# Performance work log

Measured on AMD Instinct MI355X. Metric: run time of the kernel, lower is better.

The kernel has to match this reference:

```python
import jax, jax.numpy as jnp
import numpy as np

N = 50000          # num graph nodes
E = 800000         # edges per direction
NGRAM, ODIM = 4, 32
DIMS = [128, 128, 64]
CLASSES = 128
MAXPE = 10
L2_EPS = 1e-12


def setup_inputs() -> dict:
    key = jax.random.key(0)
    ks = iter(jax.random.split(key, 40))
    d = {}
    d['x'] = jax.random.normal(next(ks), (N, DIMS[0]), jnp.float32)
    d['edge_index_in'] = jax.random.randint(next(ks), (2, E), 0, N, dtype=jnp.int64)
    d['edge_weight_in'] = jax.random.uniform(next(ks), (E,), jnp.float32)
    d['edge_index_out'] = jax.random.randint(next(ks), (2, E), 0, N, dtype=jnp.int64)
    d['edge_weight_out'] = jax.random.uniform(next(ks), (E,), jnp.float32)
    d['pe_table'] = jax.random.normal(next(ks), (MAXPE, ODIM), jnp.float32) * 0.05
    # per-layer DirectGCNLayer params (weights stored [in,out], i.e. torch W.T)
    for l in range(2):
        di, do = DIMS[l], DIMS[l + 1]
        s = 1.0 / np.sqrt(di)
        d[f'W_main_in_{l}'] = jax.random.normal(next(ks), (di, do), jnp.float32) * s
        d[f'W_main_out_{l}'] = jax.random.normal(next(ks), (di, do), jnp.float32) * s
        d[f'W_shared_{l}'] = jax.random.normal(next(ks), (di, do), jnp.float32) * s
        d[f'b_main_in_{l}'] = jnp.zeros((do,), jnp.float32)
        d[f'b_main_out_{l}'] = jnp.zeros((do,), jnp.float32)
        d[f'b_shared_in_{l}'] = jnp.zeros((do,), jnp.float32)
        d[f'b_shared_out_{l}'] = jnp.zeros((do,), jnp.float32)
        d[f'C_in_{l}'] = jnp.ones((N, 1), jnp.float32)
        d[f'C_out_{l}'] = jnp.ones((N, 1), jnp.float32)
    # residual projection for layer 1 (128 -> 64); layer 0 is identity
    d['res_W_1'] = jax.random.normal(next(ks), (DIMS[1], DIMS[2]), jnp.float32) * (1.0 / np.sqrt(DIMS[1]))
    d['res_b_1'] = jnp.zeros((DIMS[2],), jnp.float32)
    d['dec_W'] = jax.random.normal(next(ks), (DIMS[2], CLASSES), jnp.float32) * (1.0 / np.sqrt(DIMS[2]))
    d['dec_b'] = jnp.zeros((CLASSES,), jnp.float32)
    return d


def _prop(xW, ei, ew):
    # gather source, scale by edge weight, scatter-add to target (PyG aggr='add')
    return jax.ops.segment_sum(ew[:, None] * xW[ei[0]], ei[1], num_segments=N)


def _layer(h, ei_in, ew_in, ei_out, ew_out,
           Wmi, Wmo, Ws, bmi, bmo, bsi, bso, cin, cout):
    xs = h @ Ws  # shared transform, propagated over both edge sets
    ic = _prop(h @ Wmi, ei_in, ew_in) + bmi + _prop(xs, ei_in, ew_in) + bsi
    oc = _prop(h @ Wmo, ei_out, ew_out) + bmo + _prop(xs, ei_out, ew_out) + bso
    return cin * ic + cout * oc


def reference(x, edge_index_in, edge_weight_in, edge_index_out, edge_weight_out,
              pe_table,
              W_main_in_0, W_main_out_0, W_shared_0, b_main_in_0, b_main_out_0,
              b_shared_in_0, b_shared_out_0, C_in_0, C_out_0,
              W_main_in_1, W_main_out_1, W_shared_1, b_main_in_1, b_main_out_1,
              b_shared_in_1, b_shared_out_1, C_in_1, C_out_1,
              res_W_1, res_b_1, dec_W, dec_b):
    # positional encoding: add pe[:n_gram_len] to each n-gram slot
    h = (x.reshape(N, NGRAM, ODIM) + pe_table[:NGRAM][None]).reshape(N, NGRAM * ODIM)
    # layer 0 (identity residual); dropout p=0 / eval -> no-op
    h = jnp.tanh(_layer(h, edge_index_in, edge_weight_in, edge_index_out, edge_weight_out,
                        W_main_in_0, W_main_out_0, W_shared_0, b_main_in_0, b_main_out_0,
                        b_shared_in_0, b_shared_out_0, C_in_0, C_out_0) + h)
    # layer 1 (linear residual projection 128 -> 64)
    h = jnp.tanh(_layer(h, edge_index_in, edge_weight_in, edge_index_out, edge_weight_out,
                        W_main_in_1, W_main_out_1, W_shared_1, b_main_in_1, b_main_out_1,
                        b_shared_in_1, b_shared_out_1, C_in_1, C_out_1)
                 + h @ res_W_1 + res_b_1)
    logits = h @ dec_W + dec_b
    logp = jax.nn.log_softmax(logits, axis=-1)
    emb = h / (jnp.linalg.norm(h, axis=1, keepdims=True) + L2_EPS)
    return logp, emb
```

## Files before the change

### kernel.cpp

```cpp
#include <hip/hip_runtime.h>
#include <hip/hip_bf16.h>
#include <math.h>

typedef __hip_bfloat16  bf16;
typedef __hip_bfloat162 bf162;
typedef __attribute__((ext_vector_type(8))) short short8;
typedef __attribute__((ext_vector_type(4))) float floatx4;

#define BSZ     128
#define NBMAX   512
#define PACHUNK 8192

__device__ inline float4 bf4_to_f4(uint2 v) {
  float2 lo = __bfloat1622float2(*(bf162*)&v.x);
  float2 hi = __bfloat1622float2(*(bf162*)&v.y);
  return make_float4(lo.x, lo.y, hi.x, hi.y);
}
__device__ inline uint2 f4_to_bf4(float4 v) {
  bf162 lo = __float22bfloat162_rn(make_float2(v.x, v.y));
  bf162 hi = __float22bfloat162_rn(make_float2(v.z, v.w));
  uint2 r;
  r.x = *(unsigned*)&lo;
  r.y = *(unsigned*)&hi;
  return r;
}

__global__ __launch_bounds__(256) void k_bhist(const int* __restrict__ eiIn, const int* __restrict__ eiOut,
                                               int E, int* __restrict__ bcnt, int NB) {
  __shared__ int h[NBMAX];
  const int t = threadIdx.x;
  const int set = blockIdx.y;
  const int* dst = (set ? eiOut : eiIn) + E;
  for (int i = t; i < NB; i += 256) h[i] = 0;
  __syncthreads();
  const int base = blockIdx.x * PACHUNK;
  const int m = min(PACHUNK, E - base);
  #pragma unroll 4
  for (int r = 0; r < PACHUNK / 256; ++r) {
    int i = r * 256 + t;
    if (i < m) atomicAdd(&h[dst[base + i] >> 7], 1);
  }
  __syncthreads();
  for (int i = t; i < NB; i += 256) {
    int c = h[i];
    if (c) atomicAdd(&bcnt[set * NBMAX + i], c);
  }
}

__global__ __launch_bounds__(64) void k_bscan(const int* __restrict__ bcnt,
                                              int* __restrict__ BO, int* __restrict__ bcur, int NB) {
  const int set = blockIdx.x;
  const int t = threadIdx.x;
  int carry = 0;
  for (int base = 0; base < NB; base += 64) {
    int idx = base + t;
    int v = (idx < NB) ? bcnt[set * NBMAX + idx] : 0;
    int incl = v;
    #pragma unroll
    for (int d = 1; d < 64; d <<= 1) {
      int u = __shfl_up(incl, d, 64);
      if (t >= d) incl += u;
    }
    if (idx < NB) {
      int e = carry + incl - v;
      BO[set * NBMAX + idx]   = e;
      bcur[set * NBMAX + idx] = e;
    }
    carry += __shfl(incl, 63, 64);
  }
}

__global__ __launch_bounds__(256) void k_partA(const int* __restrict__ eiIn, const float* __restrict__ ewIn,
                                               const int* __restrict__ eiOut, const float* __restrict__ ewOut,
                                               int E, int* __restrict__ bucketCur,
                                               int2* __restrict__ sI, int2* __restrict__ sO, int NB) {
  __shared__ int2 staged[PACHUNK];
  __shared__ int cnt[NBMAX];
  __shared__ int sb[NBMAX];
  const int t = threadIdx.x;
  const int set = blockIdx.y;
  const int*   ei = set ? eiOut : eiIn;
  const float* ew = set ? ewOut : ewIn;
  int2* stg  = set ? sO : sI;
  int*  bcur = bucketCur + set * NBMAX;
  const int base = blockIdx.x * PACHUNK;
  const int m = min(PACHUNK, E - base);
  for (int b = t; b < NB; b += 256) cnt[b] = 0;
  __syncthreads();
  #pragma unroll 4
  for (int r = 0; r < PACHUNK / 256; ++r) {
    int i = r * 256 + t;
    if (i < m) atomicAdd(&cnt[ei[E + base + i] >> 7], 1);
  }
  __syncthreads();
  if (t < 64) {
    int carry = 0;
    int nch = (NB + 63) >> 6;
    for (int c = 0; c < nch; ++c) {
      int idx = c * 64 + t;
      int v = (idx < NB) ? cnt[idx] : 0;
      int incl = v;
      #pragma unroll
      for (int d = 1; d < 64; d <<= 1) {
        int u = __shfl_up(incl, d, 64);
        if (t >= d) incl += u;
      }
      if (idx < NB) sb[idx] = carry + incl - v;
      carry += __shfl(incl, 63, 64);
    }
  }
  __syncthreads();
  for (int b = t; b < NB; b += 256) {
    int c = cnt[b];
    if (c > 0) cnt[b] = atomicAdd(&bcur[b], c) - sb[b];
  }
  __syncthreads();
  #pragma unroll 4
  for (int r = 0; r < PACHUNK / 256; ++r) {
    int i = r * 256 + t;
    if (i < m) {
      int src = ei[base + i];
      int dst = ei[E + base + i];
      float w = ew[base + i];
      int b = dst >> 7;
      int rank = atomicAdd(&sb[b], 1);
      staged[rank] = make_int2(src | ((dst & 127) << 16) | (b << 23), __float_as_int(w));
    }
  }
  __syncthreads();
  #pragma unroll 4
  for (int r = 0; r < PACHUNK / 256; ++r) {
    int j = r * 256 + t;
    if (j < m) {
      int2 p = staged[j];
      int b = ((unsigned)p.x) >> 23;
      stg[cnt[b] + j] = p;
    }
  }
}

__global__ __launch_bounds__(256) void k_partB(const int* __restrict__ BO, const int* __restrict__ bcur,
                                               const int2* __restrict__ sI, const int2* __restrict__ sO,
                                               int2* __restrict__ eI, int2* __restrict__ eO,
                                               int* __restrict__ offsI, int* __restrict__ offsO, int N) {
  __shared__ int cnt[BSZ];
  __shared__ int excl[BSZ];
  __shared__ int cur[BSZ];
  const int t = threadIdx.x;
  const int b = blockIdx.x;
  const int set = blockIdx.y;
  const int2* stg = set ? sO : sI;
  int2* out = set ? eO : eI;
  int*  offs = set ? offsO : offsI;
  const int nlo = b << 7;
  const int nodes = min(BSZ, N - nlo);
  const int lo = BO[set * NBMAX + b];
  const int hi = bcur[set * NBMAX + b];
  if (t < BSZ) cnt[t] = 0;
  __syncthreads();
  for (int i = lo + t; i < hi; i += 256) atomicAdd(&cnt[(stg[i].x >> 16) & 127], 1);
  __syncthreads();
  if (t < 64) {
    int v0 = cnt[t];
    int i0 = v0;
    #pragma unroll
    for (int d = 1; d < 64; d <<= 1) { int u = __shfl_up(i0, d, 64); if (t >= d) i0 += u; }
    int v1 = cnt[64 + t];
    int i1 = v1;
    #pragma unroll
    for (int d = 1; d < 64; d <<= 1) { int u = __shfl_up(i1, d, 64); if (t >= d) i1 += u; }
    int tot0 = __shfl(i0, 63, 64);
    excl[t]      = i0 - v0;
    excl[64 + t] = tot0 + i1 - v1;
  }
  __syncthreads();
  if (t < BSZ) cur[t] = lo + excl[t];
  if (t < nodes) offs[nlo + t] = lo + excl[t];
  if (b == gridDim.x - 1 && t == 0) offs[N] = hi;
  __syncthreads();
  for (int i = lo + t; i < hi; i += 256) {
    int2 p = stg[i];
    int dl = (p.x >> 16) & 127;
    int pos = atomicAdd(&cur[dl], 1);
    out[pos] = make_int2(p.x & 0xffff, p.y);
  }
}

__global__ void k_wprep(const float* __restrict__ Wmi0, const float* __restrict__ Wmo0, const float* __restrict__ Ws0,
                        const float* __restrict__ Wmi1, const float* __restrict__ Wmo1, const float* __restrict__ Ws1,
                        const float* __restrict__ resW,
                        const float* __restrict__ bmi0, const float* __restrict__ bsi0,
                        const float* __restrict__ bmo0, const float* __restrict__ bso0,
                        const float* __restrict__ bmi1, const float* __restrict__ bsi1,
                        const float* __restrict__ bmo1, const float* __restrict__ bso1,
                        float* __restrict__ Wstack0, float* __restrict__ Wcat1,
                        float* __restrict__ bi0, float* __restrict__ bo0,
                        float* __restrict__ bi1, float* __restrict__ bo1) {
  int i = blockIdx.x * blockDim.x + threadIdx.x;
  if (i < 128 * 128) {
    Wstack0[i]             = Wmi0[i] + Ws0[i];
    Wstack0[128 * 128 + i] = Wmo0[i] + Ws0[i];
  }
  if (i < 128 * 192) {
    int k = i / 192, n = i % 192;
    float v;
    if (n < 64)       v = Wmi1[k * 64 + n]       + Ws1[k * 64 + n];
    else if (n < 128) v = Wmo1[k * 64 + n - 64]  + Ws1[k * 64 + n - 64];
    else              v = resW[k * 64 + n - 128];
    Wcat1[k * 192 + n] = v;
  }
  if (i < 128) { bi0[i] = bmi0[i] + bsi0[i]; bo0[i] = bmo0[i] + bso0[i]; }
  if (i < 64)  { bi1[i] = bmi1[i] + bsi1[i]; bo1[i] = bmo1[i] + bso1[i]; }
}

__device__ inline void pack_one(const float* __restrict__ W, bf16* __restrict__ P,
                                int id, int NT, int DO) {
  int lane = id & 63;
  int tile = id >> 6;
  int nt = tile % NT, kt = tile / NT;
  int col  = nt * 16 + (lane & 15);
  int krow = kt * 32 + (lane >> 4) * 8;
  bf16* dst = P + (size_t)id * 8;
  #pragma unroll
  for (int j = 0; j < 8; ++j) dst[j] = __float2bfloat16(W[(size_t)(krow + j) * DO + col]);
}
__global__ void k_packall(const float* __restrict__ W0, const float* __restrict__ W1,
                          const float* __restrict__ Wd,
                          bf16* __restrict__ P0, bf16* __restrict__ P1, bf16* __restrict__ Pd) {
  int id = blockIdx.x * blockDim.x + threadIdx.x;
  const int T0 = 8 * 8 * 64;
  const int T1 = 4 * 12 * 64;
  const int Td = 2 * 8 * 64;
  if (id < T0)                pack_one(W0, P0, id, 8, 128);
  else if (id < T0 + T1)      pack_one(W1, P1, id - T0, 12, 192);
  else if (id < T0 + T1 + Td) pack_one(Wd, Pd, id - T0 - T1, 8, 128);
}

__global__ void k_prep0(const float* __restrict__ x, const float* __restrict__ pe,
                        bf16* __restrict__ h0, int total) {
  int i = blockIdx.x * blockDim.x + threadIdx.x;
  if (i < total) h0[i] = __float2bfloat16(x[i] + pe[i & 127]);
}

__global__ __launch_bounds__(256) void k_agg0(const bf16* __restrict__ tb,
                                              const int* __restrict__ offsI, const int2* __restrict__ eI,
                                              const int* __restrict__ offsO, const int2* __restrict__ eO,
                                              const float* __restrict__ cin, const float* __restrict__ cou,
                                              bf16* __restrict__ aggC, int N) {
  int n = (blockIdx.x * blockDim.x + threadIdx.x) >> 6;
  int lane = threadIdx.x & 63;
  if (n >= N) return;
  const int sub = lane >> 5, sl = lane & 31;
  const char* base = (const char*)tb + sl * 8;
  float i0 = 0, i1 = 0, i2 = 0, i3 = 0, o0 = 0, o1 = 0, o2 = 0, o3 = 0;
  {
    int s0 = offsI[n], s1 = offsI[n + 1];
    int i = s0 + sub;
    for (; i + 6 < s1; i += 8) {
      int2 eA = eI[i], eB = eI[i + 2], eC = eI[i + 4], eD = eI[i + 6];
      float4 vA = bf4_to_f4(*(const uint2*)(base + ((size_t)(unsigned)eA.x << 8)));
      float4 vB = bf4_to_f4(*(const uint2*)(base + ((size_t)(unsigned)eB.x << 8)));
      float4 vC = bf4_to_f4(*(const uint2*)(base + ((size_t)(unsigned)eC.x << 8)));
      float4 vD = bf4_to_f4(*(const uint2*)(base + ((size_t)(unsigned)eD.x << 8)));
      float wA = __int_as_float(eA.y), wB = __int_as_float(eB.y);
      float wC = __int_as_float(eC.y), wD = __int_as_float(eD.y);
      i0 += wA * vA.x + wB * vB.x + wC * vC.x + wD * vD.x;
      i1 += wA * vA.y + wB * vB.y + wC * vC.y + wD * vD.y;
      i2 += wA * vA.z + wB * vB.z + wC * vC.z + wD * vD.z;
      i3 += wA * vA.w + wB * vB.w + wC * vC.w + wD * vD.w;
    }
    for (; i < s1; i += 2) {
      int2 e = eI[i];
      float4 v = bf4_to_f4(*(const uint2*)(base + ((size_t)(unsigned)e.x << 8)));
      float w = __int_as_float(e.y);
      i0 += w * v.x; i1 += w * v.y; i2 += w * v.z; i3 += w * v.w;
    }
  }
  {
    int s0 = offsO[n], s1 = offsO[n + 1];
    int i = s0 + sub;
    for (; i + 6 < s1; i += 8) {
      int2 eA = eO[i], eB = eO[i + 2], eC = eO[i + 4], eD = eO[i + 6];
      float4 vA = bf4_to_f4(*(const uint2*)(base + ((size_t)(unsigned)eA.x << 8)));
      float4 vB = bf4_to_f4(*(const uint2*)(base + ((size_t)(unsigned)eB.x << 8)));
      float4 vC = bf4_to_f4(*(const uint2*)(base + ((size_t)(unsigned)eC.x << 8)));
      float4 vD = bf4_to_f4(*(const uint2*)(base + ((size_t)(unsigned)eD.x << 8)));
      float wA = __int_as_float(eA.y), wB = __int_as_float(eB.y);
      float wC = __int_as_float(eC.y), wD = __int_as_float(eD.y);
      o0 += wA * vA.x + wB * vB.x + wC * vC.x + wD * vD.x;
      o1 += wA * vA.y + wB * vB.y + wC * vC.y + wD * vD.y;
      o2 += wA * vA.z + wB * vB.z + wC * vC.z + wD * vD.z;
      o3 += wA * vA.w + wB * vB.w + wC * vC.w + wD * vD.w;
    }
    for (; i < s1; i += 2) {
      int2 e = eO[i];
      float4 v = bf4_to_f4(*(const uint2*)(base + ((size_t)(unsigned)e.x << 8)));
      float w = __int_as_float(e.y);
      o0 += w * v.x; o1 += w * v.y; o2 += w * v.z; o3 += w * v.w;
    }
  }
  i0 += __shfl_xor(i0, 32, 64); i1 += __shfl_xor(i1, 32, 64);
  i2 += __shfl_xor(i2, 32, 64); i3 += __shfl_xor(i3, 32, 64);
  o0 += __shfl_xor(o0, 32, 64); o1 += __shfl_xor(o1, 32, 64);
  o2 += __shfl_xor(o2, 32, 64); o3 += __shfl_xor(o3, 32, 64);
  if (sub == 0) {
    float ci = cin[n], co = cou[n];
    *(uint2*)(aggC + (size_t)n * 256 + sl * 4)       = f4_to_bf4(make_float4(ci * i0, ci * i1, ci * i2, ci * i3));
    *(uint2*)(aggC + (size_t)n * 256 + 128 + sl * 4) = f4_to_bf4(make_float4(co * o0, co * o1, co * o2, co * o3));
  }
}

__global__ __launch_bounds__(256) void k_mf0(const bf16* __restrict__ A,
                                             const bf16* __restrict__ Wp,
                                             const float* __restrict__ bi, const float* __restrict__ bo,
                                             const float* __restrict__ cin, const float* __restrict__ cou,
                                             const bf16* __restrict__ h0,
                                             bf16* __restrict__ h1, int N) {
  const int lane = threadIdx.x & 63;
  const int quad = lane >> 4, lc = lane & 15;
  const int bmw = blockIdx.x * 64 + (threadIdx.x >> 6) * 16;
  const int rowc = min(bmw + lc, N - 1);
  const bf16* ap = A + (size_t)rowc * 256 + quad * 8;
  const short8* bp = (const short8*)Wp + lane;
  floatx4 acc[8] = {};
  #pragma unroll
  for (int kt = 0; kt < 8; ++kt) {
    short8 af = *(const short8*)(ap + kt * 32);
    #pragma unroll
    for (int nt = 0; nt < 8; ++nt) {
      short8 bfr = bp[(kt * 8 + nt) * 64];
      acc[nt] = __builtin_amdgcn_mfma_f32_16x16x32_bf16(af, bfr, acc[nt], 0, 0, 0);
    }
  }
  float bif[8], bof[8];
  #pragma unroll
  for (int nt = 0; nt < 8; ++nt) {
    bif[nt] = bi[nt * 16 + lc];
    bof[nt] = bo[nt * 16 + lc];
  }
  #pragma unroll
  for (int r = 0; r < 4; ++r) {
    int gm = bmw + quad * 4 + r;
    if (gm < N) {
      float ci = cin[gm], co = cou[gm];
      #pragma unroll
      for (int nt = 0; nt < 8; ++nt) {
        int col = nt * 16 + lc;
        float v = acc[nt][r] + ci * bif[nt] + co * bof[nt]
                + __bfloat162float(h0[(size_t)gm * 128 + col]);
        h1[(size_t)gm * 128 + col] = __float2bfloat16(tanhf(v));
      }
    }
  }
}

__global__ __launch_bounds__(256) void k_mf1(const bf16* __restrict__ A,
                                             const bf16* __restrict__ Wp,
                                             bf16* __restrict__ t1g, bf16* __restrict__ t1r, int N) {
  const int lane = threadIdx.x & 63;
  const int quad = lane >> 4, lc = lane & 15;
  const int bmw = blockIdx.x * 64 + (threadIdx.x >> 6) * 16;
  const int rowc = min(bmw + lc, N - 1);
  const bf16* ap = A + (size_t)rowc * 128 + quad * 8;
  const short8* bp = (const short8*)Wp + lane;
  floatx4 acc[12] = {};
  #pragma unroll
  for (int kt = 0; kt < 4; ++kt) {
    short8 af = *(const short8*)(ap + kt * 32);
    #pragma unroll
    for (int nt = 0; nt < 12; ++nt) {
      short8 bfr = bp[(kt * 12 + nt) * 64];
      acc[nt] = __builtin_amdgcn_mfma_f32_16x16x32_bf16(af, bfr, acc[nt], 0, 0, 0);
    }
  }
  #pragma unroll
  for (int r = 0; r < 4; ++r) {
    int gm = bmw + quad * 4 + r;
    if (gm < N) {
      #pragma unroll
      for (int nt = 0; nt < 12; ++nt) {
        int col = nt * 16 + lc;
        bf16 v = __float2bfloat16(acc[nt][r]);
        if (col < 128) t1g[(size_t)gm * 128 + col]        = v;
        else           t1r[(size_t)gm * 64 + (col - 128)] = v;
      }
    }
  }
}

__global__ __launch_bounds__(256) void k_agg1(const bf16* __restrict__ t1g, const bf16* __restrict__ t1r,
                                              const int* __restrict__ offsI, const int2* __restrict__ eI,
                                              const int* __restrict__ offsO, const int2* __restrict__ eO,
                                              const float* __restrict__ bi, const float* __restrict__ bo,
                                              const float* __restrict__ resb,
                                              const float* __restrict__ cin, const float* __restrict__ cou,
                                              bf16* __restrict__ h2b, float* __restrict__ emb, int N) {
  int n = (blockIdx.x * blockDim.x + threadIdx.x) >> 6;
  int lane = threadIdx.x & 63;
  if (n >= N) return;
  const int sub = lane >> 4;
  const int sl  = lane & 15;
  const char* baseI = (const char*)t1g + sl * 8;
  const char* baseO = baseI + 128;
  float i0 = 0, i1 = 0, i2 = 0, i3 = 0, o0 = 0, o1 = 0, o2 = 0, o3 = 0;
  {
    int s0 = offsI[n], s1 = offsI[n + 1];
    int i = s0 + sub;
    for (; i + 4 < s1; i += 8) {
      int2 eA = eI[i], eB = eI[i + 4];
      float4 vA = bf4_to_f4(*(const uint2*)(baseI + ((size_t)(unsigned)eA.x << 8)));
      float4 vB = bf4_to_f4(*(const uint2*)(baseI + ((size_t)(unsigned)eB.x << 8)));
      float wA = __int_as_float(eA.y), wB = __int_as_float(eB.y);
      i0 += wA * vA.x + wB * vB.x;
      i1 += wA * vA.y + wB * vB.y;
      i2 += wA * vA.z + wB * vB.z;
      i3 += wA * vA.w + wB * vB.w;
    }
    for (; i < s1; i += 4) {
      int2 e = eI[i];
      float4 v = bf4_to_f4(*(const uint2*)(baseI + ((size_t)(unsigned)e.x << 8)));
      float w = __int_as_float(e.y);
      i0 += w * v.x; i1 += w * v.y; i2 += w * v.z; i3 += w * v.w;
    }
  }
  {
    int s0 = offsO[n], s1 = offsO[n + 1];
    int i = s0 + sub;
    for (; i + 4 < s1; i += 8) {
      int2 eA = eO[i], eB = eO[i + 4];
      float4 vA = bf4_to_f4(*(const uint2*)(baseO + ((size_t)(unsigned)eA.x << 8)));
      float4 vB = bf4_to_f4(*(const uint2*)(baseO + ((size_t)(unsigned)eB.x << 8)));
      float wA = __int_as_float(eA.y), wB = __int_as_float(eB.y);
      o0 += wA * vA.x + wB * vB.x;
      o1 += wA * vA.y + wB * vB.y;
      o2 += wA * vA.z + wB * vB.z;
      o3 += wA * vA.w + wB * vB.w;
    }
    for (; i < s1; i += 4) {
      int2 e = eO[i];
      float4 v = bf4_to_f4(*(const uint2*)(baseO + ((size_t)(unsigned)e.x << 8)));
      float w = __int_as_float(e.y);
      o0 += w * v.x; o1 += w * v.y; o2 += w * v.z; o3 += w * v.w;
    }
  }
  i0 += __shfl_xor(i0, 32, 64); i1 += __shfl_xor(i1, 32, 64);
  i2 += __shfl_xor(i2, 32, 64); i3 += __shfl_xor(i3, 32, 64);
  o0 += __shfl_xor(o0, 32, 64); o1 += __shfl_xor(o1, 32, 64);
  o2 += __shfl_xor(o2, 32, 64); o3 += __shfl_xor(o3, 32, 64);
  i0 += __shfl_xor(i0, 16, 64); i1 += __shfl_xor(i1, 16, 64);
  i2 += __shfl_xor(i2, 16, 64); i3 += __shfl_xor(i3, 16, 64);
  o0 += __shfl_xor(o0, 16, 64); o1 += __shfl_xor(o1, 16, 64);
  o2 += __shfl_xor(o2, 16, 64); o3 += __shfl_xor(o3, 16, 64);
  if (sub == 0) {
    const int c = sl * 4;
    float ci = cin[n], co = cou[n];
    float4 bif = *(const float4*)(bi + c);
    float4 bof = *(const float4*)(bo + c);
    float4 rbf = *(const float4*)(resb + c);
    float4 rv  = bf4_to_f4(*(const uint2*)((const char*)t1r + (size_t)n * 128 + sl * 8));
    float4 v;
    v.x = tanhf(ci * (i0 + bif.x) + co * (o0 + bof.x) + rv.x + rbf.x);
    v.y = tanhf(ci * (i1 + bif.y) + co * (o1 + bof.y) + rv.y + rbf.y);
    v.z = tanhf(ci * (i2 + bif.z) + co * (o2 + bof.z) + rv.z + rbf.z);
    v.w = tanhf(ci * (i3 + bif.w) + co * (o3 + bof.w) + rv.w + rbf.w);
    *(uint2*)(h2b + (size_t)n * 64 + c) = f4_to_bf4(v);
    float q = v.x * v.x + v.y * v.y + v.z * v.z + v.w * v.w;
    #pragma unroll
    for (int d = 1; d < 16; d <<= 1) q += __shfl_xor(q, d, 64);
    float inv = 1.0f / (sqrtf(q) + 1e-12f);
    *(float4*)(emb + (size_t)n * 64 + c) = make_float4(v.x * inv, v.y * inv, v.z * inv, v.w * inv);
  }
}

__global__ __launch_bounds__(256) void k_mfd(const bf16* __restrict__ A,
                                             const bf16* __restrict__ Wp,
                                             const float* __restrict__ bd,
                                             float* __restrict__ logp, int N) {
  const int lane = threadIdx.x & 63;
  const int quad = lane >> 4, lc = lane & 15;
  const int bmw = blockIdx.x * 64 + (threadIdx.x >> 6) * 16;
  const int rowc = min(bmw + lc, N - 1);
  const bf16* ap = A + (size_t)rowc * 64 + quad * 8;
  const short8* bp = (const short8*)Wp + lane;
  floatx4 acc[8] = {};
  #pragma unroll
  for (int kt = 0; kt < 2; ++kt) {
    short8 af = *(const short8*)(ap + kt * 32);
    #pragma unroll
    for (int nt = 0; nt < 8; ++nt) {
      short8 bfr = bp[(kt * 8 + nt) * 64];
      acc[nt] = __builtin_amdgcn_mfma_f32_16x16x32_bf16(af, bfr, acc[nt], 0, 0, 0);
    }
  }
  float bdv[8];
  #pragma unroll
  for (int nt = 0; nt < 8; ++nt) bdv[nt] = bd[nt * 16 + lc];
  #pragma unroll
  for (int r = 0; r < 4; ++r) {
    int gm = bmw + quad * 4 + r;
    float v[8];
    #pragma unroll
    for (int nt = 0; nt < 8; ++nt) v[nt] = acc[nt][r] + bdv[nt];
    float m = v[0];
    #pragma unroll
    for (int nt = 1; nt < 8; ++nt) m = fmaxf(m, v[nt]);
    #pragma unroll
    for (int d = 1; d < 16; d <<= 1) m = fmaxf(m, __shfl_xor(m, d, 64));
    float s = 0.f;
    #pragma unroll
    for (int nt = 0; nt < 8; ++nt) s += __expf(v[nt] - m);
    #pragma unroll
    for (int d = 1; d < 16; d <<= 1) s += __shfl_xor(s, d, 64);
    float lse = m + __logf(s);
    if (gm < N) {
      #pragma unroll
      for (int nt = 0; nt < 8; ++nt) logp[(size_t)gm * 128 + nt * 16 + lc] = v[nt] - lse;
    }
  }
}

extern "C" void kernel_launch(void* const* d_in, const int* in_sizes, int n_in,
                              void* d_out, int out_size, void* d_ws, size_t ws_size,
                              hipStream_t stream) {
  const float* x     = (const float*)d_in[0];
  const int*   ei_in = (const int*)d_in[1];
  const float* ew_in = (const float*)d_in[2];
  const int*   ei_ou = (const int*)d_in[3];
  const float* ew_ou = (const float*)d_in[4];
  const float* pe    = (const float*)d_in[5];
  const float* Wmi0  = (const float*)d_in[6];
  const float* Wmo0  = (const float*)d_in[7];
  const float* Wsh0  = (const float*)d_in[8];
  const float* bmi0  = (const float*)d_in[9];
  const float* bmo0  = (const float*)d_in[10];
  const float* bsi0  = (const float*)d_in[11];
  const float* bso0  = (const float*)d_in[12];
  const float* cin0  = (const float*)d_in[13];
  const float* cou0  = (const float*)d_in[14];
  const float* Wmi1  = (const float*)d_in[15];
  const float* Wmo1  = (const float*)d_in[16];
  const float* Wsh1  = (const float*)d_in[17];
  const float* bmi1  = (const float*)d_in[18];
  const float* bmo1  = (const float*)d_in[19];
  const float* bsi1  = (const float*)d_in[20];
  const float* bso1  = (const float*)d_in[21];
  const float* cin1  = (const float*)d_in[22];
  const float* cou1  = (const float*)d_in[23];
  const float* resW  = (const float*)d_in[24];
  const float* resb  = (const float*)d_in[25];
  const float* Wd    = (const float*)d_in[26];
  const float* bd    = (const float*)d_in[27];

  const int N = in_sizes[0] / 128;
  const int E = in_sizes[2];
  const int NB = (N + BSZ - 1) >> 7;

  char* ws = (char*)d_ws;
  size_t off = 0;
  auto alloc = [&](size_t bytes) -> char* {
    off = (off + 255) & ~(size_t)255;
    char* p = ws + off;
    off += bytes;
    return p;
  };
  bf16*  h0bf  = (bf16*)alloc((size_t)N * 128 * 2);
  bf16*  h1bf  = (bf16*)alloc((size_t)N * 128 * 2);
  bf16*  aggC  = (bf16*)alloc((size_t)N * 256 * 2);
  bf16*  h2b   = (bf16*)alloc((size_t)N * 64 * 2);
  float* Wst0  = (float*)alloc(256 * 128 * 4);
  float* Wcat1 = (float*)alloc(128 * 192 * 4);
  bf16*  Wp0   = (bf16*)alloc(256 * 128 * 2);
  bf16*  Wp1   = (bf16*)alloc(128 * 192 * 2);
  bf16*  Wpd   = (bf16*)alloc(64 * 128 * 2);
  float* bi0   = (float*)alloc(128 * 4);
  float* bo0   = (float*)alloc(128 * 4);
  float* bi1   = (float*)alloc(64 * 4);
  float* bo1   = (float*)alloc(64 * 4);
  int*   bcnt  = (int*)alloc((size_t)2 * NBMAX * 4);
  int*   BO    = (int*)alloc((size_t)2 * NBMAX * 4);
  int*   bcur  = (int*)alloc((size_t)2 * NBMAX * 4);
  int*   offsI = (int*)alloc((size_t)(N + 1) * 4);
  int*   offsO = (int*)alloc((size_t)(N + 1) * 4);
  int2*  sI    = (int2*)alloc((size_t)E * 8);
  int2*  sO    = (int2*)alloc((size_t)E * 8);
  int2*  eI    = (int2*)alloc((size_t)E * 8);
  int2*  eO    = (int2*)alloc((size_t)E * 8);
  bf16* t1g = aggC;
  bf16* t1r = t1g + (size_t)N * 128;

  (void)hipMemsetAsync(bcnt, 0, (size_t)2 * NBMAX * 4, stream);

  dim3 gc((E + PACHUNK - 1) / PACHUNK, 2);
  k_bhist<<<gc, 256, 0, stream>>>(ei_in, ei_ou, E, bcnt, NB);
  k_bscan<<<2, 64, 0, stream>>>(bcnt, BO, bcur, NB);
  k_partA<<<gc, 256, 0, stream>>>(ei_in, ew_in, ei_ou, ew_ou, E, bcur, sI, sO, NB);
  dim3 gb(NB, 2);
  k_partB<<<gb, 256, 0, stream>>>(BO, bcur, sI, sO, eI, eO, offsI, offsO, N);
  k_wprep<<<(128 * 192 + 255) / 256, 256, 0, stream>>>(Wmi0, Wmo0, Wsh0, Wmi1, Wmo1, Wsh1, resW,
                                                       bmi0, bsi0, bmo0, bso0, bmi1, bsi1, bmo1, bso1,
                                                       Wst0, Wcat1, bi0, bo0, bi1, bo1);
  k_packall<<<(8192 + 255) / 256, 256, 0, stream>>>(Wst0, Wcat1, Wd, Wp0, Wp1, Wpd);
  k_prep0<<<(N * 128 + 255) / 256, 256, 0, stream>>>(x, pe, h0bf, N * 128);

  int ab = (N + 3) / 4;
  int mb = (N + 63) / 64;
  k_agg0<<<ab, 256, 0, stream>>>(h0bf, offsI, eI, offsO, eO, cin0, cou0, aggC, N);
  k_mf0<<<mb, 256, 0, stream>>>(aggC, Wp0, bi0, bo0, cin0, cou0, h0bf, h1bf, N);
  k_mf1<<<mb, 256, 0, stream>>>(h1bf, Wp1, t1g, t1r, N);

  float* logp = (float*)d_out;
  float* emb  = logp + (size_t)N * 128;
  k_agg1<<<ab, 256, 0, stream>>>(t1g, t1r, offsI, eI, offsO, eO, bi1, bo1, resb, cin1, cou1,
                                 h2b, emb, N);
  k_mfd<<<mb, 256, 0, stream>>>(h2b, Wpd, bd, logp, N);
}
```

Measured before the change: 373.2 us.

## Partition layer-0 aggregation by feature slice per XCD for L2 locality

Stores the layer-0 input features slice-major in four 32-column slices. The aggregation grid is remapped so each pair of XCDs gathers only one slice, keeping that slice's working set resident in its L2. Edge records are read with nontemporal 64-bit loads, and each wave handles the in and out directions in separate halves. In exchange, the edge lists are read once per slice, the source index is masked to 16 bits (valid only while N is below 65536), and the residual read in the following GEMM becomes strided.

Result: slower. 475.0 us (+27.3%).

```diff
diff --git a/kernel.cpp b/kernel.cpp
--- a/kernel.cpp
+++ b/kernel.cpp
@@ -6,10 +6,12 @@
 typedef __hip_bfloat162 bf162;
 typedef __attribute__((ext_vector_type(8))) short short8;
 typedef __attribute__((ext_vector_type(4))) float floatx4;
+typedef long long i64;
 
 #define BSZ     128
 #define NBMAX   512
 #define PACHUNK 8192
+#define NPB     128
 
 __device__ inline float4 bf4_to_f4(uint2 v) {
   float2 lo = __bfloat1622float2(*(bf162*)&v.x);
@@ -237,76 +239,68 @@
 }
 
 __global__ void k_prep0(const float* __restrict__ x, const float* __restrict__ pe,
-                        bf16* __restrict__ h0, int total) {
+                        bf16* __restrict__ h0s, int N) {
   int i = blockIdx.x * blockDim.x + threadIdx.x;
-  if (i < total) h0[i] = __float2bfloat16(x[i] + pe[i & 127]);
-}
-
-__global__ __launch_bounds__(256) void k_agg0(const bf16* __restrict__ tb,
+  if (i >= N * 128) return;
+  int c = i & 31;
+  int t = i >> 5;
+  int s = t / N;
+  int n = t - s * N;
+  int d = s * 32 + c;
+  h0s[i] = __float2bfloat16(x[(size_t)n * 128 + d] + pe[d]);
+}
+
+__global__ __launch_bounds__(256) void k_agg0(const bf16* __restrict__ tbS,
                                               const int* __restrict__ offsI, const int2* __restrict__ eI,
                                               const int* __restrict__ offsO, const int2* __restrict__ eO,
                                               const float* __restrict__ cin, const float* __restrict__ cou,
                                               bf16* __restrict__ aggC, int N) {
-  int n = (blockIdx.x * blockDim.x + threadIdx.x) >> 6;
-  int lane = threadIdx.x & 63;
-  if (n >= N) return;
-  const int sub = lane >> 5, sl = lane & 31;
-  const char* base = (const char*)tb + sl * 8;
-  float i0 = 0, i1 = 0, i2 = 0, i3 = 0, o0 = 0, o1 = 0, o2 = 0, o3 = 0;
-  {
-    int s0 = offsI[n], s1 = offsI[n + 1];
-    int i = s0 + sub;
-    for (; i + 6 < s1; i += 8) {
-      int2 eA = eI[i], eB = eI[i + 2], eC = eI[i + 4], eD = eI[i + 6];
-      float4 vA = bf4_to_f4(*(const uint2*)(base + ((size_t)(unsigned)eA.x << 8)));
-      float4 vB = bf4_to_f4(*(const uint2*)(base + ((size_t)(unsigned)eB.x << 8)));
-      float4 vC = bf4_to_f4(*(const uint2*)(base + ((size_t)(unsigned)eC.x << 8)));
-      float4 vD = bf4_to_f4(*(const uint2*)(base + ((size_t)(unsigned)eD.x << 8)));
-      float wA = __int_as_float(eA.y), wB = __int_as_float(eB.y);
-      float wC = __int_as_float(eC.y), wD = __int_as_float(eD.y);
-      i0 += wA * vA.x + wB * vB.x + wC * vC.x + wD * vD.x;
-      i1 += wA * vA.y + wB * vB.y + wC * vC.y + wD * vD.y;
-      i2 += wA * vA.z + wB * vB.z + wC * vC.z + wD * vD.z;
-      i3 += wA * vA.w + wB * vB.w + wC * vC.w + wD * vD.w;
-    }
-    for (; i < s1; i += 2) {
-      int2 e = eI[i];
-      float4 v = bf4_to_f4(*(const uint2*)(base + ((size_t)(unsigned)e.x << 8)));
-      float w = __int_as_float(e.y);
-      i0 += w * v.x; i1 += w * v.y; i2 += w * v.z; i3 += w * v.w;
-    }
-  }
-  {
-    int s0 = offsO[n], s1 = offsO[n + 1];
-    int i = s0 + sub;
-    for (; i + 6 < s1; i += 8) {
-      int2 eA = eO[i], eB = eO[i + 2], eC = eO[i + 4], eD = eO[i + 6];
-      float4 vA = bf4_to_f4(*(const uint2*)(base + ((size_t)(unsigned)eA.x << 8)));
-      float4 vB = bf4_to_f4(*(const uint2*)(base + ((size_t)(unsigned)eB.x << 8)));
-      float4 vC = bf4_to_f4(*(const uint2*)(base + ((size_t)(unsigned)eC.x << 8)));
-      float4 vD = bf4_to_f4(*(const uint2*)(base + ((size_t)(unsigned)eD.x << 8)));
-      float wA = __int_as_float(eA.y), wB = __int_as_float(eB.y);
-      float wC = __int_as_float(eC.y), wD = __int_as_float(eD.y);
-      o0 += wA * vA.x + wB * vB.x + wC * vC.x + wD * vD.x;
-      o1 += wA * vA.y + wB * vB.y + wC * vC.y + wD * vD.y;
-      o2 += wA * vA.z + wB * vB.z + wC * vC.z + wD * vD.z;
-      o3 += wA * vA.w + wB * vB.w + wC * vC.w + wD * vD.w;
-    }
-    for (; i < s1; i += 2) {
-      int2 e = eO[i];
-      float4 v = bf4_to_f4(*(const uint2*)(base + ((size_t)(unsigned)e.x << 8)));
-      float w = __int_as_float(e.y);
-      o0 += w * v.x; o1 += w * v.y; o2 += w * v.z; o3 += w * v.w;
-    }
-  }
-  i0 += __shfl_xor(i0, 32, 64); i1 += __shfl_xor(i1, 32, 64);
-  i2 += __shfl_xor(i2, 32, 64); i3 += __shfl_xor(i3, 32, 64);
-  o0 += __shfl_xor(o0, 32, 64); o1 += __shfl_xor(o1, 32, 64);
-  o2 += __shfl_xor(o2, 32, 64); o3 += __shfl_xor(o3, 32, 64);
-  if (sub == 0) {
-    float ci = cin[n], co = cou[n];
-    *(uint2*)(aggC + (size_t)n * 256 + sl * 4)       = f4_to_bf4(make_float4(ci * i0, ci * i1, ci * i2, ci * i3));
-    *(uint2*)(aggC + (size_t)n * 256 + 128 + sl * 4) = f4_to_bf4(make_float4(co * o0, co * o1, co * o2, co * o3));
+  const int b     = blockIdx.x;
+  const int xcd   = b & 7;
+  const int slice = xcd >> 1;
+  const int half  = xcd & 1;
+  const int worker = (b >> 3) * 2 + half;
+  const int lane = threadIdx.x & 63;
+  const int w    = threadIdx.x >> 6;
+  const int dir  = lane >> 5;
+  const int eu   = (lane >> 3) & 3;
+  const int le   = lane & 7;
+  const int*   offs = dir ? offsO : offsI;
+  const int2*  el   = dir ? eO : eI;
+  const float* cc   = dir ? cou : cin;
+  const char* tb = (const char*)tbS + (size_t)slice * N * 64 + le * 8;
+  int n0 = worker * NPB + w * (NPB / 4);
+  int n1 = min(n0 + NPB / 4, N);
+  for (int n = n0; n < n1; ++n) {
+    int s0 = offs[n], s1 = offs[n + 1];
+    float a0 = 0, a1 = 0, a2 = 0, a3 = 0;
+    int i = s0 + eu;
+    for (; i + 4 < s1; i += 8) {
+      i64 pA = __builtin_nontemporal_load((const i64*)(el + i));
+      i64 pB = __builtin_nontemporal_load((const i64*)(el + i + 4));
+      float4 vA = bf4_to_f4(*(const uint2*)(tb + ((size_t)(unsigned)(pA & 0xffff) << 6)));
+      float4 vB = bf4_to_f4(*(const uint2*)(tb + ((size_t)(unsigned)(pB & 0xffff) << 6)));
+      float wA = __int_as_float((int)(pA >> 32)), wB = __int_as_float((int)(pB >> 32));
+      a0 += wA * vA.x + wB * vB.x;
+      a1 += wA * vA.y + wB * vB.y;
+      a2 += wA * vA.z + wB * vB.z;
+      a3 += wA * vA.w + wB * vB.w;
+    }
+    for (; i < s1; i += 4) {
+      i64 p = __builtin_nontemporal_load((const i64*)(el + i));
+      float4 v = bf4_to_f4(*(const uint2*)(tb + ((size_t)(unsigned)(p & 0xffff) << 6)));
+      float wv = __int_as_float((int)(p >> 32));
+      a0 += wv * v.x; a1 += wv * v.y; a2 += wv * v.z; a3 += wv * v.w;
+    }
+    a0 += __shfl_xor(a0, 8, 64);  a1 += __shfl_xor(a1, 8, 64);
+    a2 += __shfl_xor(a2, 8, 64);  a3 += __shfl_xor(a3, 8, 64);
+    a0 += __shfl_xor(a0, 16, 64); a1 += __shfl_xor(a1, 16, 64);
+    a2 += __shfl_xor(a2, 16, 64); a3 += __shfl_xor(a3, 16, 64);
+    if (eu == 0) {
+      float c = cc[n];
+      *(uint2*)(aggC + (size_t)n * 256 + dir * 128 + slice * 32 + le * 4)
+        = f4_to_bf4(make_float4(c * a0, c * a1, c * a2, c * a3));
+    }
   }
 }
 
@@ -347,7 +341,7 @@
       for (int nt = 0; nt < 8; ++nt) {
         int col = nt * 16 + lc;
         float v = acc[nt][r] + ci * bif[nt] + co * bof[nt]
-                + __bfloat162float(h0[(size_t)gm * 128 + col]);
+                + __bfloat162float(h0[((size_t)(col >> 5) * N + gm) * 32 + (col & 31)]);
         h1[(size_t)gm * 128 + col] = __float2bfloat16(tanhf(v));
       }
     }
@@ -600,11 +594,13 @@
                                                        bmi0, bsi0, bmo0, bso0, bmi1, bsi1, bmo1, bso1,
                                                        Wst0, Wcat1, bi0, bo0, bi1, bo1);
   k_packall<<<(8192 + 255) / 256, 256, 0, stream>>>(Wst0, Wcat1, Wd, Wp0, Wp1, Wpd);
-  k_prep0<<<(N * 128 + 255) / 256, 256, 0, stream>>>(x, pe, h0bf, N * 128);
+  k_prep0<<<(N * 128 + 255) / 256, 256, 0, stream>>>(x, pe, h0bf, N);
 
   int ab = (N + 3) / 4;
   int mb = (N + 63) / 64;
-  k_agg0<<<ab, 256, 0, stream>>>(h0bf, offsI, eI, offsO, eO, cin0, cou0, aggC, N);
+  int nw = (N + NPB - 1) / NPB;
+  int gj = (nw + 1) / 2;
+  k_agg0<<<gj * 8, 256, 0, stream>>>(h0bf, offsI, eI, offsO, eO, cin0, cou0, aggC, N);
   k_mf0<<<mb, 256, 0, stream>>>(aggC, Wp0, bi0, bo0, cin0, cou0, h0bf, h1bf, N);
   k_mf1<<<mb, 256, 0, stream>>>(h1bf, Wp1, t1g, t1r, N);
 
```
